# Kernel optimization log

Hardware: AMD Instinct MI355X
Metric: run time of the kernel (lower is better)

## Reference

```python
import jax, jax.numpy as jnp
import numpy as np

B, C, K, T = 8, 256, 64, 1000
NORM_EPS = 1e-12


def setup_inputs() -> dict:
    key = jax.random.key(0)
    k_x, k_codes, k_scales = jax.random.split(key, 3)
    init_val = 1.0 / (K * C) ** 0.5
    x = jax.random.normal(k_x, (B, C, T), dtype=jnp.float32)
    codes = jax.random.uniform(k_codes, (C, K), dtype=jnp.float32,
                               minval=-init_val, maxval=init_val)
    scales = jax.random.uniform(k_scales, (K,), dtype=jnp.float32,
                                minval=0.0, maxval=1.0)
    return {"x": x, "codes": codes, "scales": scales}


def l2_normalize(t, axis, eps=NORM_EPS):
    n = jnp.sqrt(jnp.sum(t * t, axis=axis, keepdims=True))
    n = jnp.maximum(n, eps)
    return t / n


def reference(x, codes, scales):
    # x: (B, C, T); codes: (C, K); scales: (K,)
    residual = x[:, :, None, :] - codes[None, :, :, None]      # (B, C, K, T)
    residual_l2sqr = jnp.sum(residual * residual, axis=1)      # (B, K, T)
    weights_tc = jax.nn.softmax(-scales[None, :, None] * residual_l2sqr, axis=1)  # softmax over codes K
    embeddings = jnp.einsum('bckt,bkt->bkc', residual, weights_tc) / x.shape[-1]  # (B, K, C)
    embeddings = l2_normalize(embeddings, axis=-1)
    return embeddings
```

## Files before the change

kernel.cpp:

```cpp
#include <hip/hip_runtime.h>
#include <stdint.h>

constexpr int Bn  = 8;
constexpr int Cn  = 256;
constexpr int Kn  = 64;
constexpr int Tn  = 1000;
constexpr int CH  = 32;
constexpr int NCH = 32;

constexpr int XT_P = 264;
constexpr int XC_P = 40;
constexpr int MW_P = 33;
constexpr int WL_P = 40;

typedef float f32x4 __attribute__((ext_vector_type(4)));
typedef __bf16 bf16x8 __attribute__((ext_vector_type(8)));

__device__ __forceinline__ unsigned short f2bf(float f) {
    unsigned u = __float_as_uint(f);
    return (unsigned short)((u + 0x7FFFu + ((u >> 16) & 1u)) >> 16);
}

union BF8 { unsigned short u[8]; bf16x8 v; };

__global__ __launch_bounds__(512, 2) void lde_wp(
    const float* __restrict__ x,
    const float* __restrict__ codes,
    const float* __restrict__ scales,
    float* __restrict__ part,
    float* __restrict__ Sp)
{
    __shared__ __align__(16) unsigned short xT[CH * XT_P];
    __shared__ __align__(16) unsigned short xc[Cn * XC_P];
    __shared__ __align__(16) unsigned short wl[Kn * WL_P];
    __shared__ float Mw[Kn * MW_P];
    __shared__ float xsqp[64 * 33];
    __shared__ float xsq[CH];
    __shared__ float csqs[Kn];
    __shared__ float spw[8 * 64];

    const int tid  = threadIdx.x;
    const int wave = tid >> 6;
    const int lane = tid & 63;
    const int n    = lane & 15;
    const int q    = lane >> 4;
    const int b    = blockIdx.x >> 5;
    const int ch   = blockIdx.x & 31;
    const int t0   = ch * CH;
    const float sc = scales[lane];

    {
        const int tf = tid & 7;
        const int cg = tid >> 3;
        const float* xb = x + (size_t)b * Cn * Tn;
        float s0 = 0.f, s1 = 0.f, s2 = 0.f, s3 = 0.f;
        const int t = t0 + 4 * tf;
#pragma unroll
        for (int r = 0; r < 4; ++r) {
            int c = cg + 64 * r;
            float4 v;
            if (t + 3 < Tn) {
                v = *(const float4*)(xb + (size_t)c * Tn + t);
            } else {
                v.x = (t     < Tn) ? xb[(size_t)c * Tn + t]     : 0.f;
                v.y = (t + 1 < Tn) ? xb[(size_t)c * Tn + t + 1] : 0.f;
                v.z = (t + 2 < Tn) ? xb[(size_t)c * Tn + t + 2] : 0.f;
                v.w = (t + 3 < Tn) ? xb[(size_t)c * Tn + t + 3] : 0.f;
            }
            unsigned short h0 = f2bf(v.x), h1 = f2bf(v.y);
            unsigned short h2 = f2bf(v.z), h3 = f2bf(v.w);
            xT[(4 * tf + 0) * XT_P + c] = h0;
            xT[(4 * tf + 1) * XT_P + c] = h1;
            xT[(4 * tf + 2) * XT_P + c] = h2;
            xT[(4 * tf + 3) * XT_P + c] = h3;
            *(ushort4*)(xc + c * XC_P + 4 * tf) = make_ushort4(h0, h1, h2, h3);
            s0 = fmaf(v.x, v.x, s0);
            s1 = fmaf(v.y, v.y, s1);
            s2 = fmaf(v.z, v.z, s2);
            s3 = fmaf(v.w, v.w, s3);
        }
        float* xp = xsqp + cg * 33 + 4 * tf;
        xp[0] = s0; xp[1] = s1; xp[2] = s2; xp[3] = s3;
    }
    __syncthreads();

    if (tid < 32) {
        float a = 0.f;
#pragma unroll
        for (int g = 0; g < 64; ++g) a += xsqp[g * 33 + tid];
        xsq[tid] = a;
    }

    {
        const int kt    = wave >> 1;
        const int tt    = wave & 1;
        const int kglob = kt * 16 + n;
        const float* cod = codes + (size_t)(q * 8) * Kn + kglob;
        float csq_part = 0.f;
        f32x4 acc = {0.f, 0.f, 0.f, 0.f};
#pragma unroll
        for (int c0 = 0; c0 < Cn; c0 += 32) {
            float cf[8];
#pragma unroll
            for (int j = 0; j < 8; ++j) cf[j] = cod[(size_t)(c0 + j) * Kn];
            BF8 aF;
#pragma unroll
            for (int j = 0; j < 8; ++j) {
                csq_part = fmaf(cf[j], cf[j], csq_part);
                aF.u[j] = f2bf(cf[j]);
            }
            bf16x8 bF = *(const bf16x8*)(xT + (tt * 16 + n) * XT_P + c0 + q * 8);
            acc = __builtin_amdgcn_mfma_f32_16x16x32_bf16(aF.v, bF, acc, 0, 0, 0);
        }
        csq_part += __shfl_xor(csq_part, 16, 64);
        csq_part += __shfl_xor(csq_part, 32, 64);
        if (tt == 0 && q == 0) csqs[kglob] = csq_part;
#pragma unroll
        for (int r = 0; r < 4; ++r)
            Mw[(kt * 16 + q * 4 + r) * MW_P + tt * 16 + n] = acc[r];
    }
    __syncthreads();

    {
        const float cq = csqs[lane];
        float sp = 0.f;
#pragma unroll
        for (int j = 0; j < 4; ++j) {
            int t = 4 * wave + j;
            float m     = Mw[lane * MW_P + t];
            float logit = -sc * (xsq[t] - 2.f * m + cq);
            float mx = logit;
#pragma unroll
            for (int off = 32; off >= 1; off >>= 1)
                mx = fmaxf(mx, __shfl_xor(mx, off, 64));
            float e = __expf(logit - mx);
            float s = e;
#pragma unroll
            for (int off = 32; off >= 1; off >>= 1)
                s += __shfl_xor(s, off, 64);
            float wv = e / s;
            if (t0 + t >= Tn) wv = 0.f;
            sp += wv;
            wl[lane * WL_P + t] = f2bf(wv);
        }
        spw[wave * 64 + lane] = sp;
    }
    __syncthreads();

    if (tid < 64) {
        float s = 0.f;
#pragma unroll
        for (int w = 0; w < 8; ++w) s += spw[w * 64 + tid];
        Sp[((size_t)b * Kn + tid) * NCH + ch] = s;
    }

    {
        const int kt    = wave >> 1;
        const int chalf = (wave & 1) * 128;
        bf16x8 aF = *(const bf16x8*)(wl + (kt * 16 + n) * WL_P + q * 8);
        float* pb0 = part + ((size_t)(b * NCH + ch) * Kn + kt * 16 + q * 4) * Cn;
#pragma unroll
        for (int s = 0; s < 8; ++s) {
            int cc = chalf + s * 16;
            bf16x8 bF = *(const bf16x8*)(xc + (cc + n) * XC_P + q * 8);
            f32x4 acc = {0.f, 0.f, 0.f, 0.f};
            acc = __builtin_amdgcn_mfma_f32_16x16x32_bf16(aF, bF, acc, 0, 0, 0);
#pragma unroll
            for (int r = 0; r < 4; ++r)
                pb0[(size_t)r * Cn + cc + n] = acc[r];
        }
    }
}

__global__ __launch_bounds__(256) void lde_fin(
    const float* __restrict__ part,
    const float* __restrict__ Sp,
    const float* __restrict__ codes,
    float* __restrict__ out)
{
    const int b    = blockIdx.x >> 6;
    const int k    = blockIdx.x & 63;
    const int tid  = threadIdx.x;
    const int lane = tid & 63;
    const int wave = tid >> 6;

    __shared__ float red[4];
    __shared__ float Ss;

    if (wave == 0) {
        float s = (lane < NCH) ? Sp[((size_t)b * Kn + k) * NCH + lane] : 0.f;
#pragma unroll
        for (int off = 32; off >= 1; off >>= 1) s += __shfl_xor(s, off, 64);
        if (lane == 0) Ss = s;
    }
    __syncthreads();
    const float S = Ss;

    const int c = tid;
    const float* pb = part + (size_t)b * NCH * Kn * Cn + (size_t)k * Cn + c;
    float val = 0.f;
#pragma unroll
    for (int chn = 0; chn < NCH; ++chn) val += pb[(size_t)chn * Kn * Cn];

    float e = (val - codes[c * Kn + k] * S) * (1.0f / (float)Tn);

    float qq = e * e;
#pragma unroll
    for (int off = 32; off >= 1; off >>= 1) qq += __shfl_xor(qq, off, 64);
    if (lane == 0) red[wave] = qq;
    __syncthreads();
    float nn = sqrtf(red[0] + red[1] + red[2] + red[3]);

    out[((size_t)b * Kn + k) * Cn + c] = e / fmaxf(nn, 1e-12f);
}

extern "C" void kernel_launch(void* const* d_in, const int* in_sizes, int n_in,
                              void* d_out, int out_size, void* d_ws, size_t ws_size,
                              hipStream_t stream) {
    const float* x      = (const float*)d_in[0];
    const float* codes  = (const float*)d_in[1];
    const float* scales = (const float*)d_in[2];
    float* out = (float*)d_out;

    char* ws = (char*)d_ws;
    float* part = (float*)ws;
    float* Sp   = (float*)(ws + (16u << 20));

    lde_wp <<<Bn * NCH, 512, 0, stream>>>(x, codes, scales, part, Sp);
    lde_fin<<<Bn * Kn,  256, 0, stream>>>(part, Sp, codes, out);
}
```

Baseline: 76.39 us.

## Fuse finalize pass into main kernel via cooperative grid sync

Merges the two-kernel pipeline into one cooperative launch: after computing per-chunk partials, all blocks hit a grid-wide barrier, then each block finalizes two (b,k) rows (reduce partials, subtract code term, L2 normalize). This removes a second kernel launch and its scheduling gap, at the cost of a grid barrier and a cooperative-launch requirement that all 256 blocks be co-resident.

New measurement: 126.0 us. 1.65x slower.

```diff
diff --git a/kernel.cpp b/kernel.cpp
--- a/kernel.cpp
+++ b/kernel.cpp
@@ -1,5 +1,8 @@
 #include <hip/hip_runtime.h>
+#include <hip/hip_cooperative_groups.h>
 #include <stdint.h>
+
+namespace cg = cooperative_groups;
 
 constexpr int Bn  = 8;
 constexpr int Cn  = 256;
@@ -23,12 +26,13 @@
 
 union BF8 { unsigned short u[8]; bf16x8 v; };
 
-__global__ __launch_bounds__(512, 2) void lde_wp(
+__global__ __launch_bounds__(512, 2) void lde_all(
     const float* __restrict__ x,
     const float* __restrict__ codes,
     const float* __restrict__ scales,
     float* __restrict__ part,
-    float* __restrict__ Sp)
+    float* __restrict__ Sp,
+    float* __restrict__ out)
 {
     __shared__ __align__(16) unsigned short xT[CH * XT_P];
     __shared__ __align__(16) unsigned short xc[Cn * XC_P];
@@ -38,6 +42,7 @@
     __shared__ float xsq[CH];
     __shared__ float csqs[Kn];
     __shared__ float spw[8 * 64];
+    __shared__ float red2[8];
 
     const int tid  = threadIdx.x;
     const int wave = tid >> 6;
@@ -170,48 +175,39 @@
                 pb0[(size_t)r * Cn + cc + n] = acc[r];
         }
     }
-}
-
-__global__ __launch_bounds__(256) void lde_fin(
-    const float* __restrict__ part,
-    const float* __restrict__ Sp,
-    const float* __restrict__ codes,
-    float* __restrict__ out)
-{
-    const int b    = blockIdx.x >> 6;
-    const int k    = blockIdx.x & 63;
-    const int tid  = threadIdx.x;
-    const int lane = tid & 63;
-    const int wave = tid >> 6;
-
-    __shared__ float red[4];
-    __shared__ float Ss;
-
-    if (wave == 0) {
-        float s = (lane < NCH) ? Sp[((size_t)b * Kn + k) * NCH + lane] : 0.f;
+
+    cg::this_grid().sync();
+
+    {
+        const int h  = tid >> 8;
+        const int c  = tid & 255;
+        const int bk = 2 * (int)blockIdx.x + h;
+        const int b2 = bk >> 6;
+        const int k2 = bk & 63;
+        const int l  = tid & 63;
+
+        float s = (l < NCH) ? Sp[(size_t)bk * NCH + l] : 0.f;
 #pragma unroll
         for (int off = 32; off >= 1; off >>= 1) s += __shfl_xor(s, off, 64);
-        if (lane == 0) Ss = s;
-    }
-    __syncthreads();
-    const float S = Ss;
-
-    const int c = tid;
-    const float* pb = part + (size_t)b * NCH * Kn * Cn + (size_t)k * Cn + c;
-    float val = 0.f;
-#pragma unroll
-    for (int chn = 0; chn < NCH; ++chn) val += pb[(size_t)chn * Kn * Cn];
-
-    float e = (val - codes[c * Kn + k] * S) * (1.0f / (float)Tn);
-
-    float qq = e * e;
-#pragma unroll
-    for (int off = 32; off >= 1; off >>= 1) qq += __shfl_xor(qq, off, 64);
-    if (lane == 0) red[wave] = qq;
-    __syncthreads();
-    float nn = sqrtf(red[0] + red[1] + red[2] + red[3]);
-
-    out[((size_t)b * Kn + k) * Cn + c] = e / fmaxf(nn, 1e-12f);
+        const float S = s;
+
+        const float* pb = part + ((size_t)b2 * NCH * Kn + k2) * Cn + c;
+        float val = 0.f;
+#pragma unroll
+        for (int ch2 = 0; ch2 < NCH; ++ch2) val += pb[(size_t)ch2 * Kn * Cn];
+
+        float e = (val - codes[c * Kn + k2] * S) * (1.0f / (float)Tn);
+
+        float qq = e * e;
+#pragma unroll
+        for (int off = 32; off >= 1; off >>= 1) qq += __shfl_xor(qq, off, 64);
+        if (l == 0) red2[tid >> 6] = qq;
+        __syncthreads();
+        const int hw = h * 4;
+        float nn = sqrtf(red2[hw] + red2[hw + 1] + red2[hw + 2] + red2[hw + 3]);
+
+        out[(size_t)bk * Cn + c] = e / fmaxf(nn, 1e-12f);
+    }
 }
 
 extern "C" void kernel_launch(void* const* d_in, const int* in_sizes, int n_in,
@@ -226,6 +222,8 @@
     float* part = (float*)ws;
     float* Sp   = (float*)(ws + (16u << 20));
 
-    lde_wp <<<Bn * NCH, 512, 0, stream>>>(x, codes, scales, part, Sp);
-    lde_fin<<<Bn * Kn,  256, 0, stream>>>(part, Sp, codes, out);
+    void* args[] = { (void*)&x, (void*)&codes, (void*)&scales,
+                     (void*)&part, (void*)&Sp, (void*)&out };
+    hipLaunchCooperativeKernel((void*)lde_all, dim3(Bn * NCH), dim3(512),
+                               args, 0, stream);
 }
```

## Split each time-chunk across two 256-thread blocks with XCD-aware block mapping

Applied to the files above, without the earlier changes.

Doubles the grid of the weight/partial kernel to 512 blocks of 256 threads. The two blocks sharing a time chunk each redundantly compute the distance GEMM and softmax, then each writes half of the channel dimension of the partial embeddings. Block indices are remapped so both halves of a chunk land on the same XCD, letting the shared x reads hit in L2. The aim is more blocks and better CU occupancy across the device, at the cost of duplicated x loads, distance MFMAs and softmax work.

Measured after the change: 77.74 us. No clear change (+1.8%).

```diff
diff --git a/kernel.cpp b/kernel.cpp
--- a/kernel.cpp
+++ b/kernel.cpp
@@ -23,7 +23,7 @@
 
 union BF8 { unsigned short u[8]; bf16x8 v; };
 
-__global__ __launch_bounds__(512, 2) void lde_wp(
+__global__ __launch_bounds__(256, 4) void lde_wp(
     const float* __restrict__ x,
     const float* __restrict__ codes,
     const float* __restrict__ scales,
@@ -31,23 +31,28 @@
     float* __restrict__ Sp)
 {
     __shared__ __align__(16) unsigned short xT[CH * XT_P];
-    __shared__ __align__(16) unsigned short xc[Cn * XC_P];
+    __shared__ __align__(16) unsigned short xc[128 * XC_P];
     __shared__ __align__(16) unsigned short wl[Kn * WL_P];
     __shared__ float Mw[Kn * MW_P];
-    __shared__ float xsqp[64 * 33];
+    __shared__ float xsqp[32 * 33];
     __shared__ float xsq[CH];
     __shared__ float csqs[Kn];
-    __shared__ float spw[8 * 64];
+    __shared__ float spw[4 * 64];
 
     const int tid  = threadIdx.x;
     const int wave = tid >> 6;
     const int lane = tid & 63;
     const int n    = lane & 15;
     const int q    = lane >> 4;
-    const int b    = blockIdx.x >> 5;
-    const int ch   = blockIdx.x & 31;
-    const int t0   = ch * CH;
-    const float sc = scales[lane];
+
+    const int bid   = (int)blockIdx.x;
+    const int xcd   = bid & 7;
+    const int half  = (bid >> 3) & 1;
+    const int chunk = (bid >> 4) * 8 + xcd;
+    const int b     = chunk >> 5;
+    const int ch    = chunk & 31;
+    const int t0    = ch * CH;
+    const float sc  = scales[lane];
 
     {
         const int tf = tid & 7;
@@ -56,8 +61,8 @@
         float s0 = 0.f, s1 = 0.f, s2 = 0.f, s3 = 0.f;
         const int t = t0 + 4 * tf;
 #pragma unroll
-        for (int r = 0; r < 4; ++r) {
-            int c = cg + 64 * r;
+        for (int r = 0; r < 8; ++r) {
+            int c = cg + 32 * r;
             float4 v;
             if (t + 3 < Tn) {
                 v = *(const float4*)(xb + (size_t)c * Tn + t);
@@ -73,7 +78,11 @@
             xT[(4 * tf + 1) * XT_P + c] = h1;
             xT[(4 * tf + 2) * XT_P + c] = h2;
             xT[(4 * tf + 3) * XT_P + c] = h3;
-            *(ushort4*)(xc + c * XC_P + 4 * tf) = make_ushort4(h0, h1, h2, h3);
+            if ((r >> 2) == half) {
+                int cl = cg + 32 * (r & 3);
+                *(ushort4*)(xc + cl * XC_P + 4 * tf) =
+                    make_ushort4(h0, h1, h2, h3);
+            }
             s0 = fmaf(v.x, v.x, s0);
             s1 = fmaf(v.y, v.y, s1);
             s2 = fmaf(v.z, v.z, s2);
@@ -87,17 +96,17 @@
     if (tid < 32) {
         float a = 0.f;
 #pragma unroll
-        for (int g = 0; g < 64; ++g) a += xsqp[g * 33 + tid];
+        for (int g = 0; g < 32; ++g) a += xsqp[g * 33 + tid];
         xsq[tid] = a;
     }
 
     {
-        const int kt    = wave >> 1;
-        const int tt    = wave & 1;
+        const int kt    = wave;
         const int kglob = kt * 16 + n;
         const float* cod = codes + (size_t)(q * 8) * Kn + kglob;
         float csq_part = 0.f;
-        f32x4 acc = {0.f, 0.f, 0.f, 0.f};
+        f32x4 acc0 = {0.f, 0.f, 0.f, 0.f};
+        f32x4 acc1 = {0.f, 0.f, 0.f, 0.f};
 #pragma unroll
         for (int c0 = 0; c0 < Cn; c0 += 32) {
             float cf[8];
@@ -109,15 +118,19 @@
                 csq_part = fmaf(cf[j], cf[j], csq_part);
                 aF.u[j] = f2bf(cf[j]);
             }
-            bf16x8 bF = *(const bf16x8*)(xT + (tt * 16 + n) * XT_P + c0 + q * 8);
-            acc = __builtin_amdgcn_mfma_f32_16x16x32_bf16(aF.v, bF, acc, 0, 0, 0);
+            bf16x8 b0 = *(const bf16x8*)(xT + n * XT_P + c0 + q * 8);
+            bf16x8 b1 = *(const bf16x8*)(xT + (16 + n) * XT_P + c0 + q * 8);
+            acc0 = __builtin_amdgcn_mfma_f32_16x16x32_bf16(aF.v, b0, acc0, 0, 0, 0);
+            acc1 = __builtin_amdgcn_mfma_f32_16x16x32_bf16(aF.v, b1, acc1, 0, 0, 0);
         }
         csq_part += __shfl_xor(csq_part, 16, 64);
         csq_part += __shfl_xor(csq_part, 32, 64);
-        if (tt == 0 && q == 0) csqs[kglob] = csq_part;
-#pragma unroll
-        for (int r = 0; r < 4; ++r)
-            Mw[(kt * 16 + q * 4 + r) * MW_P + tt * 16 + n] = acc[r];
+        if (q == 0) csqs[kglob] = csq_part;
+#pragma unroll
+        for (int r = 0; r < 4; ++r) {
+            Mw[(kt * 16 + q * 4 + r) * MW_P + n]      = acc0[r];
+            Mw[(kt * 16 + q * 4 + r) * MW_P + 16 + n] = acc1[r];
+        }
     }
     __syncthreads();
 
@@ -125,8 +138,8 @@
         const float cq = csqs[lane];
         float sp = 0.f;
 #pragma unroll
-        for (int j = 0; j < 4; ++j) {
-            int t = 4 * wave + j;
+        for (int j = 0; j < 8; ++j) {
+            int t = 8 * wave + j;
             float m     = Mw[lane * MW_P + t];
             float logit = -sc * (xsq[t] - 2.f * m + cq);
             float mx = logit;
@@ -147,27 +160,24 @@
     }
     __syncthreads();
 
-    if (tid < 64) {
-        float s = 0.f;
-#pragma unroll
-        for (int w = 0; w < 8; ++w) s += spw[w * 64 + tid];
+    if (half == 0 && tid < 64) {
+        float s = spw[tid] + spw[64 + tid] + spw[128 + tid] + spw[192 + tid];
         Sp[((size_t)b * Kn + tid) * NCH + ch] = s;
     }
 
     {
-        const int kt    = wave >> 1;
-        const int chalf = (wave & 1) * 128;
+        const int kt = wave;
         bf16x8 aF = *(const bf16x8*)(wl + (kt * 16 + n) * WL_P + q * 8);
-        float* pb0 = part + ((size_t)(b * NCH + ch) * Kn + kt * 16 + q * 4) * Cn;
+        float* pb0 = part + ((size_t)(b * NCH + ch) * Kn + kt * 16 + q * 4) * Cn
+                   + half * 128;
 #pragma unroll
         for (int s = 0; s < 8; ++s) {
-            int cc = chalf + s * 16;
-            bf16x8 bF = *(const bf16x8*)(xc + (cc + n) * XC_P + q * 8);
+            bf16x8 bF = *(const bf16x8*)(xc + (s * 16 + n) * XC_P + q * 8);
             f32x4 acc = {0.f, 0.f, 0.f, 0.f};
             acc = __builtin_amdgcn_mfma_f32_16x16x32_bf16(aF, bF, acc, 0, 0, 0);
 #pragma unroll
             for (int r = 0; r < 4; ++r)
-                pb0[(size_t)r * Cn + cc + n] = acc[r];
+                pb0[(size_t)r * Cn + s * 16 + n] = acc[r];
         }
     }
 }
@@ -226,6 +236,6 @@
     float* part = (float*)ws;
     float* Sp   = (float*)(ws + (16u << 20));
 
-    lde_wp <<<Bn * NCH, 512, 0, stream>>>(x, codes, scales, part, Sp);
-    lde_fin<<<Bn * Kn,  256, 0, stream>>>(part, Sp, codes, out);
-}
+    lde_wp <<<2 * Bn * NCH, 256, 0, stream>>>(x, codes, scales, part, Sp);
+    lde_fin<<<Bn * Kn,      256, 0, stream>>>(part, Sp, codes, out);
+}
```
